# Kernel tuning notes

Measured on AMD Instinct MI355X. Metric: run time of the kernel, lower is better.

The kernel has to match this reference:

```python
import jax, jax.numpy as jnp
import numpy as np

NUM_CLASSES = 4
TRAIN_SWITCH = True
TOPO = {1: {0: 1, 1: 0}, 2: {0: 1, 1: 1}, 3: {0: 2, 1: 0}, 4: {0: 1, 1: 0}}


def _sublevel_h0(v, H, W, eight):
    """0-dim sublevel-set persistence of a 2D grid via union-find.

    v: flat numpy array of length H*W. eight: 8-connectivity (gudhi
    T-construction, lower cells = min of cofaces) vs 4-connectivity (dual).
    Returns (pairs, essential_idx): pairs is a list of (birth_idx, death_idx)
    pixel indices with strictly positive persistence; essential_idx is the
    pixel index of the global-min (essential, death = +inf) component.
    """
    N = H * W
    order = np.argsort(v, kind='stable')
    rank = np.empty(N, np.int64)
    rank[order] = np.arange(N)
    parent = np.full(N, -1, np.int64)   # -1 = not yet in filtration
    creator = np.zeros(N, np.int64)     # pixel realizing the component's birth
    pairs = []

    def find(a):
        root = a
        while parent[root] != root:
            root = parent[root]
        while parent[a] != root:
            parent[a], a = root, parent[a]
        return root

    offs = [(-1, 0), (1, 0), (0, -1), (0, 1)]
    if eight:
        offs += [(-1, -1), (-1, 1), (1, -1), (1, 1)]
    for idx in order:
        idx = int(idx)
        r, c = divmod(idx, W)
        parent[idx] = idx
        creator[idx] = idx
        for dr, dc in offs:
            rr, cc = r + dr, c + dc
            if 0 <= rr < H and 0 <= cc < W:
                nb = rr * W + cc
                if parent[nb] >= 0:
                    ra, rb = find(idx), find(nb)
                    if ra != rb:
                        # elder rule: component with earlier (smaller) birth survives
                        if rank[creator[ra]] < rank[creator[rb]]:
                            elder, young = ra, rb
                        else:
                            elder, young = rb, ra
                        if v[idx] > v[creator[young]]:  # drop 0-persistence pairs (gudhi default)
                            pairs.append((int(creator[young]), idx))
                        parent[young] = elder
    ess = int(creator[find(int(order[0]))])
    return pairs, ess


def _diagrams(img):
    """H0 and H1 persistence pairs (as pixel indices) of a 2D image,
    matching gudhi.CubicalComplex(top_dimensional_cells=img).persistence().
    H0: sublevel union-find with 8-connectivity. H1 by Alexander duality:
    superlevel H0 with 4-connectivity, pairs reversed."""
    H, W = img.shape
    v = img.ravel()
    h0, ess = _sublevel_h0(v, H, W, eight=True)
    sup, _ = _sublevel_h0(-v, H, W, eight=False)
    h1 = [(d, b) for (b, d) in sup]  # (saddle birth, max death)
    pers = lambda p: v[p[1]] - v[p[0]]
    h0.sort(key=pers, reverse=True)  # gudhi orders by decreasing persistence
    h1.sort(key=pers, reverse=True)
    return h0, ess, h1


def _dim_loss(flat, pairs, ess_idx, nf):
    """loss_per_dimension: first nf pairs are 'kept' -> (1-pers)^2, missing
    features cost 1 each, extra pairs cost pers^2. Essential (death=inf)
    pair has pers = 1 - birth and sorts first (infinite persistence)."""
    parts = []
    if ess_idx is not None:
        parts.append((1.0 - flat[ess_idx])[None])
    if pairs:
        b = np.asarray([p[0] for p in pairs], np.int64)
        d = np.asarray([p[1] for p in pairs], np.int64)
        parts.append(flat[d] - flat[b])
    pvec = jnp.concatenate(parts) if parts else jnp.zeros((0,), flat.dtype)
    n = pvec.shape[0]
    return jnp.sum((1.0 - pvec[:nf]) ** 2) + float(max(0, nf - n)) + jnp.sum(pvec[nf:] ** 2)


def setup_inputs() -> dict:
    key = jax.random.key(0)
    # (1, batch, classes, H, W); values in [0,1] like softmax probabilities
    x = jax.random.uniform(key, (1, 4, NUM_CLASSES, 64, 64), dtype=jnp.float32)
    return {"x": x}


def reference(x):
    xs = x[0]  # squeeze(0) -> (B, C, H, W)
    if not TRAIN_SWITCH:
        xs = jnp.clip(1.0 - xs, 0.0, 1.0)
    xn = np.asarray(xs)
    B, C, H, W = xn.shape
    loss = jnp.zeros((), jnp.float32)
    for b in range(B):
        for c in range(1, C):  # skip background class 0
            h0, ess, h1 = _diagrams(xn[b, c])
            flat = xs[b, c].ravel()
            loss = loss + _dim_loss(flat, h0, ess, TOPO[c][0])
            loss = loss + _dim_loss(flat, h1, None, TOPO[c][1])
    return loss / B
```

## Files before the change

### kernel.cpp

```cpp
#include <hip/hip_runtime.h>

#define NPIX 4096
#define NT 1024
#define PPT (NPIX / NT)
#define EMPTY 0xFFFFFFFFu
#define FLAGMAGIC 0x00C0FFEEu

__global__ void ph_zero_kernel(float* out) { out[0] = 0.0f; }

__device__ __forceinline__ float kval(unsigned k) {
  unsigned u = (k & 0x80000000u) ? (k & 0x7FFFFFFFu) : ~k;
  return __uint_as_float(u);
}

__global__ __launch_bounds__(NT) void ph_pass_kernel(const float* __restrict__ x,
                                                     float* __restrict__ out,
                                                     unsigned long long* __restrict__ ws64,
                                                     int use_ws) {
  __shared__ unsigned long long pool[2 * NPIX];
  __shared__ unsigned long long claim64[NPIX];
  __shared__ unsigned long long wred[32];
  __shared__ int s_chg[13];
  __shared__ int s_flag;
  __shared__ double s_sum[16];
  __shared__ float s_max[16];
  __shared__ int s_cnt[16];

  unsigned long long* sbuf = pool;
  unsigned* hkey = (unsigned*)pool;
  unsigned* hval = hkey + NPIX;
  unsigned* key32 = (unsigned*)(pool + NPIX);
  unsigned short* label = (unsigned short*)(pool + NPIX + NPIX / 2);
  unsigned long long* node = pool + NPIX;

  const int blk = blockIdx.x;
  const int b = blk / 6;
  const int rem = blk % 6;
  const int c = (rem >> 1) + 1;
  const int pass = rem & 1;
  const float* img = x + (size_t)(b * 4 + c) * NPIX;
  const int tid = threadIdx.x;
  const int lane = tid & 63, wid = tid >> 6;
  const int ndirs = pass ? 4 : 8;
  const int drr[8] = {-1, 1, 0, 0, -1, -1, 1, 1};
  const int dcc[8] = { 0, 0,-1, 1, -1,  1, -1, 1};

  if (tid < 13) s_chg[tid] = 0;
  unsigned lmin = EMPTY;
  for (int i = tid; i < NPIX; i += NT) {
    float f = img[i];
    if (pass) f = -f;
    unsigned u = __float_as_uint(f);
    unsigned k = (u & 0x80000000u) ? ~u : (u | 0x80000000u);
    key32[i] = k;
    pool[i] = ~0ull;
    claim64[i] = 0ull;
    lmin = min(lmin, k);
  }
  for (int off = 32; off > 0; off >>= 1)
    lmin = min(lmin, (unsigned)__shfl_xor((int)lmin, off));
  if (lane == 0) wred[wid] = lmin;
  __syncthreads();
  unsigned vmink = (unsigned)wred[0];
  #pragma unroll
  for (int w = 1; w < 16; w++) vmink = min(vmink, (unsigned)wred[w]);

  for (int i = tid; i < NPIX; i += NT) {
    unsigned long long best = ((unsigned long long)key32[i] << 32) | (unsigned)i;
    int bestnb = i;
    int r = i >> 6, cc = i & 63;
    for (int d = 0; d < ndirs; d++) {
      int rr = r + drr[d], c2 = cc + dcc[d];
      if ((unsigned)rr >= 64u || (unsigned)c2 >= 64u) continue;
      int nb = (rr << 6) | c2;
      unsigned long long pn = ((unsigned long long)key32[nb] << 32) | (unsigned)nb;
      if (pn < best) { best = pn; bestnb = nb; }
    }
    label[i] = (unsigned short)bestnb;
  }
  __syncthreads();
  for (int round = 0; round < 12; round++) {
    bool changed = false;
    for (int i = tid; i < NPIX; i += NT) {
      unsigned short l = label[i];
      unsigned short l2 = label[l];
      if (l2 != l) { label[i] = l2; changed = true; }
    }
    if (changed) s_chg[round] = 1;
    __syncthreads();
    if (!s_chg[round]) break;
  }

  const int pdr[4] = {1, 0, 1,  1};
  const int pdc[4] = {0, 1, 1, -1};
  const int npd = pass ? 2 : 4;
  for (int i = tid; i < NPIX; i += NT) {
    int r = i >> 6, cc = i & 63;
    unsigned la = label[i];
    unsigned ki = key32[i];
    for (int d = 0; d < npd; d++) {
      int rr = r + pdr[d], c2 = cc + pdc[d];
      if ((unsigned)rr >= 64u || (unsigned)c2 >= 64u) continue;
      int nb = (rr << 6) | c2;
      unsigned lb = label[nb];
      if (lb == la) continue;
      unsigned wkey = max(ki, key32[nb]);
      unsigned pk = la < lb ? ((la << 12) | lb) : ((lb << 12) | la);
      unsigned h = (pk * 2654435761u) >> 20;
      while (true) {
        unsigned old = atomicCAS(&hkey[h], EMPTY, pk);
        if (old == EMPTY || old == pk) { atomicMin(&hval[h], wkey); break; }
        h = (h + 1) & (NPIX - 1);
      }
    }
  }
  __syncthreads();

  unsigned long long item[PPT];
  unsigned mykeys[PPT];
  int cnt = 0;
  #pragma unroll
  for (int q = 0; q < PPT; q++) {
    int s = tid * PPT + q;
    unsigned pk = hkey[s];
    if (pk != EMPTY) item[cnt++] = (((unsigned long long)hval[s]) << 32) | pk;
  }
  #pragma unroll
  for (int t = 0; t < PPT; t++) mykeys[t] = key32[tid + t * NT];
  __syncthreads();
  unsigned inc = (unsigned)cnt;
  for (int off = 1; off < 64; off <<= 1) {
    unsigned v = __shfl_up(inc, off);
    if (lane >= off) inc += v;
  }
  if (lane == 63) wred[wid] = inc;
  __syncthreads();
  if (wid == 0) {
    unsigned wv = (lane < 16) ? (unsigned)wred[lane] : 0u;
    for (int off = 1; off < 16; off <<= 1) {
      unsigned v = __shfl_up(wv, off);
      if (lane >= off) wv += v;
    }
    if (lane < 16) wred[16 + lane] = wv;
  }
  __syncthreads();
  const int M = (int)wred[31];
  const int base0 = (int)((wid ? (unsigned)wred[16 + wid - 1] : 0u) + inc) - cnt;
  for (int q = 0; q < cnt; q++) sbuf[base0 + q] = item[q];
  #pragma unroll
  for (int t = 0; t < PPT; t++) {
    int i = tid + t * NT;
    node[i] = (((unsigned long long)mykeys[t]) << 32) | (unsigned)i;
  }
  __syncthreads();

  double sumsq = 0.0;
  float maxp = 0.0f;
  int pcnt = 0;
  unsigned ewk[PPT], exa[PPT], exb[PPT];
  unsigned long long erA[PPT], erB[PPT];
  unsigned pmask = 0;
  #pragma unroll
  for (int q = 0; q < PPT; q++) {
    const int j = tid + q * NT;
    if (j < M) {
      const unsigned long long e = sbuf[j];
      ewk[q] = (unsigned)(e >> 32);
      const unsigned pk = (unsigned)(e & 0xFFFFFFu);
      unsigned xa = pk >> 12, xb = pk & 0xFFFu;
      unsigned long long recA = node[xa], recB = node[xb];
      while ((unsigned)recA != xa) { xa = (unsigned)recA; recA = node[xa]; }
      while ((unsigned)recB != xb) { xb = (unsigned)recB; recB = node[xb]; }
      exa[q] = xa; exb[q] = xb; erA[q] = recA; erB[q] = recB;
      if (xa != xb) pmask |= 1u << q;
    }
  }
  unsigned long long seqtag = 0;
  while (true) {
    seqtag += (1ull << 44);
    #pragma unroll
    for (int q = 0; q < PPT; q++) {
      if (pmask & (1u << q)) {
        const int j = tid + q * NT;
        const unsigned long long myval =
            seqtag | (((unsigned long long)(~ewk[q])) << 12) | (unsigned)j;
        unsigned young, elder;
        if (erA[q] < erB[q]) { elder = exa[q]; young = exb[q]; }
        else                 { elder = exb[q]; young = exa[q]; }
        atomicMax(&claim64[young], myval);
        atomicMax(&claim64[elder], myval);
      }
    }
    __syncthreads();
    if (tid == 0) s_flag = 0;
    #pragma unroll
    for (int q = 0; q < PPT; q++) {
      if (pmask & (1u << q)) {
        const int j = tid + q * NT;
        const unsigned long long myval =
            seqtag | (((unsigned long long)(~ewk[q])) << 12) | (unsigned)j;
        unsigned young, elder;
        unsigned long long yrec;
        if (erA[q] < erB[q]) { elder = exa[q]; young = exb[q]; yrec = erB[q]; }
        else                 { elder = exb[q]; young = exa[q]; yrec = erA[q]; }
        if (claim64[young] == myval) {
          const unsigned ky = (unsigned)(yrec >> 32);
          if (ewk[q] > ky) {
            float pers = kval(ewk[q]) - kval(ky);
            sumsq += (double)pers * (double)pers;
            maxp = fmaxf(maxp, pers);
            pcnt++;
          }
          node[young] = (yrec & 0xFFFFFFFF00000000ull) | elder;
          pmask &= ~(1u << q);
        }
      }
    }
    __syncthreads();
    bool any = false;
    #pragma unroll
    for (int q = 0; q < PPT; q++) {
      if (pmask & (1u << q)) {
        unsigned xa = exa[q], xb = exb[q];
        unsigned long long recA = node[xa], recB = node[xb];
        while ((unsigned)recA != xa) { xa = (unsigned)recA; recA = node[xa]; }
        while ((unsigned)recB != xb) { xb = (unsigned)recB; recB = node[xb]; }
        exa[q] = xa; exb[q] = xb; erA[q] = recA; erB[q] = recB;
        if (xa == xb) pmask &= ~(1u << q);
        else any = true;
      }
    }
    if (any) s_flag = 1;
    __syncthreads();
    if (!s_flag) break;
  }
  for (int off = 32; off > 0; off >>= 1) {
    sumsq += __shfl_xor(sumsq, off);
    maxp = fmaxf(maxp, __shfl_xor(maxp, off));
    pcnt += __shfl_xor(pcnt, off);
  }
  if (lane == 0) { s_sum[wid] = sumsq; s_max[wid] = maxp; s_cnt[wid] = pcnt; }
  __syncthreads();

  float contrib = 0.0f;
  if (tid == 0) {
    #pragma unroll
    for (int w = 1; w < 16; w++) {
      sumsq += s_sum[w];
      maxp = fmaxf(maxp, s_max[w]);
      pcnt += s_cnt[w];
    }
    if (pass == 0) {
      const int nf0 = (c == 3) ? 2 : 1;
      float vmin = kval(vmink);
      if (nf0 == 1) {
        contrib = vmin * vmin + (float)sumsq;
      } else if (pcnt >= 1) {
        contrib = vmin * vmin + (1.0f - maxp) * (1.0f - maxp)
                + (float)(sumsq - (double)maxp * (double)maxp);
      } else {
        contrib = vmin * vmin + 1.0f;
      }
    } else {
      const int nf1 = (c == 2) ? 1 : 0;
      if (nf1 == 0) contrib = (float)sumsq;
      else contrib = (pcnt >= 1)
        ? ((1.0f - maxp) * (1.0f - maxp) + (float)(sumsq - (double)maxp * (double)maxp))
        : 1.0f;
    }
    contrib *= 0.25f;
    if (use_ws) {
      atomicExch(&ws64[blk],
                 (((unsigned long long)__float_as_uint(contrib)) << 32) | FLAGMAGIC);
    } else {
      atomicAdd(out, contrib);
    }
  }
  if (use_ws && blk == 0 && wid == 0) {
    float v = 0.0f;
    if (lane < 24) {
      while (true) {
        unsigned long long r = atomicAdd(&ws64[lane], 0ull);
        if ((unsigned)r == FLAGMAGIC) { v = __uint_as_float((unsigned)(r >> 32)); break; }
      }
    }
    for (int off = 32; off > 0; off >>= 1) v += __shfl_xor(v, off);
    if (lane == 0) out[0] = v;
  }
}

extern "C" void kernel_launch(void* const* d_in, const int* in_sizes, int n_in,
                              void* d_out, int out_size, void* d_ws, size_t ws_size,
                              hipStream_t stream) {
  const float* x = (const float*)d_in[0];
  float* out = (float*)d_out;
  if (ws_size >= 24 * sizeof(unsigned long long)) {
    ph_pass_kernel<<<24, NT, 0, stream>>>(x, out, (unsigned long long*)d_ws, 1);
  } else {
    ph_zero_kernel<<<1, 1, 0, stream>>>(out);
    ph_pass_kernel<<<24, NT, 0, stream>>>(x, out, nullptr, 0);
  }
}
```

Measured before the change: 92.48 us.

## Merge union-find claim and find phases to cut barriers per round

The parallel union-find merge loop now issues the next round's atomic claims in the same phase as the root re-find. A double-buffered shared flag replaces the separate flag reset and extra barrier, so each round needs two barriers instead of three. The initial root-finding is skipped because every edge's endpoints start as their own roots. The label pointer-jumping also does four hops per round, with at most six rounds, and atomics are skipped when the current claim is already larger. The risks are correctness subtleties in the reordered flag protocol and a possibly changed number of rounds.

Result: no change. 94.32 us (+2.0%).

```diff
diff --git a/kernel.cpp b/kernel.cpp
--- a/kernel.cpp
+++ b/kernel.cpp
@@ -21,7 +21,6 @@
   __shared__ unsigned long long claim64[NPIX];
   __shared__ unsigned long long wred[32];
   __shared__ int s_chg[13];
-  __shared__ int s_flag;
   __shared__ double s_sum[16];
   __shared__ float s_max[16];
   __shared__ int s_cnt[16];
@@ -79,12 +78,14 @@
     label[i] = (unsigned short)bestnb;
   }
   __syncthreads();
-  for (int round = 0; round < 12; round++) {
+  for (int round = 0; round < 6; round++) {
     bool changed = false;
     for (int i = tid; i < NPIX; i += NT) {
       unsigned short l = label[i];
       unsigned short l2 = label[l];
-      if (l2 != l) { label[i] = l2; changed = true; }
+      unsigned short l3 = label[l2];
+      unsigned short l4 = label[l3];
+      if (l4 != l) { label[i] = l4; changed = true; }
     }
     if (changed) s_chg[round] = 1;
     __syncthreads();
@@ -152,6 +153,7 @@
     int i = tid + t * NT;
     node[i] = (((unsigned long long)mykeys[t]) << 32) | (unsigned)i;
   }
+  if (tid < 2) s_chg[tid] = 0;
   __syncthreads();
 
   double sumsq = 0.0;
@@ -168,31 +170,28 @@
       ewk[q] = (unsigned)(e >> 32);
       const unsigned pk = (unsigned)(e & 0xFFFFFFu);
       unsigned xa = pk >> 12, xb = pk & 0xFFFu;
-      unsigned long long recA = node[xa], recB = node[xb];
-      while ((unsigned)recA != xa) { xa = (unsigned)recA; recA = node[xa]; }
-      while ((unsigned)recB != xb) { xb = (unsigned)recB; recB = node[xb]; }
-      exa[q] = xa; exb[q] = xb; erA[q] = recA; erB[q] = recB;
-      if (xa != xb) pmask |= 1u << q;
-    }
-  }
-  unsigned long long seqtag = 0;
+      exa[q] = xa; exb[q] = xb;
+      erA[q] = node[xa]; erB[q] = node[xb];
+      pmask |= 1u << q;
+    }
+  }
+  unsigned long long seqtag = (1ull << 44);
+  #pragma unroll
+  for (int q = 0; q < PPT; q++) {
+    if (pmask & (1u << q)) {
+      const int j = tid + q * NT;
+      const unsigned long long myval =
+          seqtag | (((unsigned long long)(~ewk[q])) << 12) | (unsigned)j;
+      unsigned young, elder;
+      if (erA[q] < erB[q]) { elder = exa[q]; young = exb[q]; }
+      else                 { elder = exb[q]; young = exa[q]; }
+      if (claim64[young] < myval) atomicMax(&claim64[young], myval);
+      if (claim64[elder] < myval) atomicMax(&claim64[elder], myval);
+    }
+  }
+  int rt = 1;
   while (true) {
-    seqtag += (1ull << 44);
-    #pragma unroll
-    for (int q = 0; q < PPT; q++) {
-      if (pmask & (1u << q)) {
-        const int j = tid + q * NT;
-        const unsigned long long myval =
-            seqtag | (((unsigned long long)(~ewk[q])) << 12) | (unsigned)j;
-        unsigned young, elder;
-        if (erA[q] < erB[q]) { elder = exa[q]; young = exb[q]; }
-        else                 { elder = exb[q]; young = exa[q]; }
-        atomicMax(&claim64[young], myval);
-        atomicMax(&claim64[elder], myval);
-      }
-    }
     __syncthreads();
-    if (tid == 0) s_flag = 0;
     #pragma unroll
     for (int q = 0; q < PPT; q++) {
       if (pmask & (1u << q)) {
@@ -216,8 +215,11 @@
         }
       }
     }
+    if (pmask) s_chg[rt & 1] = 1;
+    if (tid == 0) s_chg[(rt + 1) & 1] = 0;
     __syncthreads();
-    bool any = false;
+    if (!s_chg[rt & 1]) break;
+    rt++; seqtag += (1ull << 44);
     #pragma unroll
     for (int q = 0; q < PPT; q++) {
       if (pmask & (1u << q)) {
@@ -226,13 +228,20 @@
         while ((unsigned)recA != xa) { xa = (unsigned)recA; recA = node[xa]; }
         while ((unsigned)recB != xb) { xb = (unsigned)recB; recB = node[xb]; }
         exa[q] = xa; exb[q] = xb; erA[q] = recA; erB[q] = recB;
-        if (xa == xb) pmask &= ~(1u << q);
-        else any = true;
-      }
-    }
-    if (any) s_flag = 1;
-    __syncthreads();
-    if (!s_flag) break;
+        if (xa == xb) {
+          pmask &= ~(1u << q);
+        } else {
+          const int j = tid + q * NT;
+          const unsigned long long myval =
+              seqtag | (((unsigned long long)(~ewk[q])) << 12) | (unsigned)j;
+          unsigned young, elder;
+          if (recA < recB) { elder = xa; young = xb; }
+          else             { elder = xb; young = xa; }
+          if (claim64[young] < myval) atomicMax(&claim64[young], myval);
+          if (claim64[elder] < myval) atomicMax(&claim64[elder], myval);
+        }
+      }
+    }
   }
   for (int off = 32; off > 0; off >>= 1) {
     sumsq += __shfl_xor(sumsq, off);
```
